# Performance work log

Hardware: AMD Instinct MI355X
Metric: run time of the kernel (lower is better)

The kernel has to match this reference:

```python
import jax, jax.numpy as jnp
import numpy as np

N, M = 1024, 1024
GATES = ["ii", "hi", "if", "hf", "ig", "hg", "io", "ho"]


def setup_inputs() -> dict:
    key = jax.random.key(0)
    names = ["x", "h", "c"] + [f"{p}_{g}" for g in GATES for p in ("L", "R", "b")]
    keys = jax.random.split(key, len(names))
    out = {}
    for nm, k in zip(names, keys):
        if nm in ("x", "h", "c"):
            sh = (N, M)
            scale = 1.0
        else:
            p = nm.split("_")[0]
            sh = {"L": (N, N), "R": (M, M), "b": (N, M)}[p]
            scale = 0.05  # keep gate pre-activations in a sane range
        out[nm] = jax.random.normal(k, sh, dtype=jnp.float32) * scale
    return out


def _klin(L, R, b, x):
    # kronecker_addmm: left @ x @ right + bias
    return L @ x @ R + b


def reference(x, h, c,
              L_ii, R_ii, b_ii, L_hi, R_hi, b_hi,
              L_if, R_if, b_if, L_hf, R_hf, b_hf,
              L_ig, R_ig, b_ig, L_hg, R_hg, b_hg,
              L_io, R_io, b_io, L_ho, R_ho, b_ho):
    i = jax.nn.sigmoid(_klin(L_ii, R_ii, b_ii, x) + _klin(L_hi, R_hi, b_hi, h))
    f = jax.nn.sigmoid(_klin(L_if, R_if, b_if, x) + _klin(L_hf, R_hf, b_hf, h))
    g = jnp.tanh(_klin(L_ig, R_ig, b_ig, x) + _klin(L_hg, R_hg, b_hg, h))
    o = jax.nn.sigmoid(_klin(L_io, R_io, b_io, x) + _klin(L_ho, R_ho, b_ho, h))
    c_new = f * c + i * g
    h_new = o * jnp.tanh(c_new)
    return (h_new, c_new)
```

## Files before the change

### kernel.cpp

```cpp
#include <hip/hip_runtime.h>
#include <stdint.h>

typedef __bf16 bf16x8 __attribute__((ext_vector_type(8)));
typedef float  f32x4  __attribute__((ext_vector_type(4)));
typedef uint16_t u16;

#define MAT_ELEMS (1024 * 1024)
#define LDK 1024


__device__ __forceinline__ u16 to_bf16(float f) {
  union { float f; uint32_t u; } v; v.f = f;
  uint32_t u = v.u;
  uint32_t r = u + 0x7FFFu + ((u >> 16) & 1u);
  return (u16)(r >> 16);
}

__device__ __forceinline__ void gll16(const void* g, void* l) {
  __builtin_amdgcn_global_load_lds(
      (__attribute__((address_space(1))) void*)const_cast<void*>(g),
      (__attribute__((address_space(3))) void*)(l),
      16, 0, 0);
}

__device__ __forceinline__ float fast_sigmoid(float x) {
  x = fminf(fmaxf(x, -30.f), 30.f);
  return 1.0f / (1.0f + __expf(-x));
}

__device__ __forceinline__ float fast_tanh(float x) {
  x = fminf(fmaxf(x, -15.f), 15.f);
  float e = __expf(2.0f * x);
  return (e - 1.0f) / (e + 1.0f);
}


struct P8  { const float* p[8]; };
struct P10 { const float* p[10]; };
struct B8  { const float* b[8]; };

__global__ __launch_bounds__(256) void cast8_kernel(P8 s, u16* __restrict__ dst) {
  const float* src = s.p[blockIdx.y];
  u16* d = dst + ((size_t)blockIdx.y << 20);
  int i = (blockIdx.x * 256 + threadIdx.x) * 4;
  f32x4 v = *reinterpret_cast<const f32x4*>(src + i);
  ushort4 o;
  o.x = to_bf16(v[0]); o.y = to_bf16(v[1]);
  o.z = to_bf16(v[2]); o.w = to_bf16(v[3]);
  *reinterpret_cast<ushort4*>(d + i) = o;
}

__global__ __launch_bounds__(256) void transpose_cast_kernel(P10 s, u16* __restrict__ dstbase) {
  __shared__ float tile[32][33];
  const float* src = s.p[blockIdx.z];
  u16* dst = dstbase + ((size_t)blockIdx.z << 20);
  int tx = threadIdx.x & 31;
  int ty = threadIdx.x >> 5;
  int c0 = blockIdx.x * 32;
  int r0 = blockIdx.y * 32;
#pragma unroll
  for (int i = 0; i < 4; ++i)
    tile[ty + i * 8][tx] = src[(size_t)(r0 + ty + i * 8) * 1024 + c0 + tx];
  __syncthreads();
#pragma unroll
  for (int i = 0; i < 4; ++i) {
    int n = c0 + ty + i * 8;
    int k = r0 + tx;
    dst[(size_t)n * 1024 + k] = to_bf16(tile[tx][ty + i * 8]);
  }
}


template <int MODE>
__device__ __forceinline__ void gemm_body(
    const u16* __restrict__ A0, const u16* __restrict__ A1,
    const u16* __restrict__ B0, const u16* __restrict__ B1,
    int nkt, int kt_split, int row0, int col0,
    u16* __restrict__ outb, float* __restrict__ outf,
    const float* __restrict__ bias0, const float* __restrict__ bias1,
    u16* As, u16* Bs)
{
  const int tid  = threadIdx.x;
  const int lane = tid & 63;
  const int w    = tid >> 6;
  const int wr   = w >> 1;
  const int wc   = w & 1;
  const int r16  = lane & 15;
  const int kg   = lane >> 4;

  f32x4 acc[4][4];
#pragma unroll
  for (int m = 0; m < 4; ++m)
#pragma unroll
    for (int n = 0; n < 4; ++n) {
      f32x4 z = {0.f, 0.f, 0.f, 0.f};
      acc[m][n] = z;
    }

  const int srow = tid >> 2;
  const int skk  = (tid & 3) * 8;
  u16* lA0 = As + srow * 32 + skk;
  u16* lA1 = As + (srow + 64) * 32 + skk;
  u16* lB0 = Bs + srow * 32 + skk;
  u16* lB1 = Bs + (srow + 64) * 32 + skk;

  for (int kt = 0; kt < nkt; ++kt) {
    const u16* Ak = (kt < kt_split) ? (A0 + kt * 32) : (A1 + (kt - kt_split) * 32);
    const u16* Bk = (kt < kt_split) ? (B0 + kt * 32) : (B1 + (kt - kt_split) * 32);
    __syncthreads();
    gll16(Ak + (size_t)(row0 + srow)      * LDK + skk, lA0);
    gll16(Ak + (size_t)(row0 + srow + 64) * LDK + skk, lA1);
    gll16(Bk + (size_t)(col0 + srow)      * LDK + skk, lB0);
    gll16(Bk + (size_t)(col0 + srow + 64) * LDK + skk, lB1);
    __syncthreads();

    bf16x8 af[4], bfr[4];
#pragma unroll
    for (int m = 0; m < 4; ++m)
      af[m] = *reinterpret_cast<const bf16x8*>(As + (wr * 64 + m * 16 + r16) * 32 + kg * 8);
#pragma unroll
    for (int n = 0; n < 4; ++n)
      bfr[n] = *reinterpret_cast<const bf16x8*>(Bs + (wc * 64 + n * 16 + r16) * 32 + kg * 8);
#pragma unroll
    for (int m = 0; m < 4; ++m)
#pragma unroll
      for (int n = 0; n < 4; ++n)
        acc[m][n] = __builtin_amdgcn_mfma_f32_16x16x32_bf16(af[m], bfr[n], acc[m][n], 0, 0, 0);
  }

#pragma unroll
  for (int m = 0; m < 4; ++m) {
#pragma unroll
    for (int r = 0; r < 4; ++r) {
      int row = row0 + wr * 64 + m * 16 + kg * 4 + r;
#pragma unroll
      for (int n = 0; n < 4; ++n) {
        int col = col0 + wc * 64 + n * 16 + r16;
        if (MODE == 0) {
          outb[(size_t)row * 1024 + col] = to_bf16(acc[m][n][r]);
        } else {
          size_t idx = (size_t)row * 1024 + col;
          outf[idx] = acc[m][n][r] + bias0[idx] + bias1[idx];
        }
      }
    }
  }
}

__global__ __launch_bounds__(256) void gemm_stage1_kernel(
    const u16* __restrict__ Lb, const u16* __restrict__ xT,
    const u16* __restrict__ hT, u16* __restrict__ Tbuf)
{
  __shared__ u16 As[128 * 32];
  __shared__ u16 Bs[128 * 32];
  int g = blockIdx.y;
  const u16* A = Lb + ((size_t)g << 20);
  const u16* B = (g & 1) ? hT : xT;
  u16* out = Tbuf + ((size_t)g << 20);
  int row0 = (blockIdx.x >> 3) * 128;
  int col0 = (blockIdx.x & 7) * 128;
  gemm_body<0>(A, A, B, B, 32, 32, row0, col0, out, nullptr, nullptr, nullptr, As, Bs);
}

__global__ __launch_bounds__(256) void gemm_stage2_kernel(
    const u16* __restrict__ Tbuf, const u16* __restrict__ RT,
    B8 bp, float* __restrict__ P)
{
  __shared__ u16 As[128 * 32];
  __shared__ u16 Bs[128 * 32];
  int j = blockIdx.y;
  const u16* A0 = Tbuf + ((size_t)(2 * j) << 20);
  const u16* B0 = RT   + ((size_t)(2 * j) << 20);
  int row0 = (blockIdx.x >> 3) * 128;
  int col0 = (blockIdx.x & 7) * 128;
  gemm_body<1>(A0, A0 + MAT_ELEMS, B0, B0 + MAT_ELEMS, 64, 32, row0, col0,
               nullptr, P + ((size_t)j << 20), bp.b[2 * j], bp.b[2 * j + 1], As, Bs);
}

__global__ __launch_bounds__(256) void lstm_cell_kernel(
    const float* __restrict__ P, const float* __restrict__ c, float* __restrict__ out)
{
  int i = (blockIdx.x * 256 + threadIdx.x) * 4;
  f32x4 pi = *reinterpret_cast<const f32x4*>(P + i);
  f32x4 pf = *reinterpret_cast<const f32x4*>(P + MAT_ELEMS + i);
  f32x4 pg = *reinterpret_cast<const f32x4*>(P + 2 * MAT_ELEMS + i);
  f32x4 po = *reinterpret_cast<const f32x4*>(P + 3 * MAT_ELEMS + i);
  f32x4 cc = *reinterpret_cast<const f32x4*>(c + i);
  f32x4 hn, cn;
#pragma unroll
  for (int j = 0; j < 4; ++j) {
    float ig = fast_sigmoid(pi[j]);
    float fg = fast_sigmoid(pf[j]);
    float gg = fast_tanh(pg[j]);
    float og = fast_sigmoid(po[j]);
    float cv = fg * cc[j] + ig * gg;
    cn[j] = cv;
    hn[j] = og * fast_tanh(cv);
  }
  *reinterpret_cast<f32x4*>(out + i) = hn;
  *reinterpret_cast<f32x4*>(out + MAT_ELEMS + i) = cn;
}


extern "C" void kernel_launch(void* const* d_in, const int* in_sizes, int n_in,
                              void* d_out, int out_size, void* d_ws, size_t ws_size,
                              hipStream_t stream) {
  const float* x = (const float*)d_in[0];
  const float* h = (const float*)d_in[1];
  const float* c = (const float*)d_in[2];

  u16* Lb   = (u16*)d_ws;
  u16* xT   = Lb + ((size_t)8 << 20);
  u16* hT   = xT + ((size_t)1 << 20);
  u16* RT   = hT + ((size_t)1 << 20);
  u16* Tbuf = RT + ((size_t)8 << 20);
  float* P  = (float*)(Tbuf + ((size_t)8 << 20));

  P8 lp;
  for (int g = 0; g < 8; ++g) lp.p[g] = (const float*)d_in[3 + 3 * g];
  P10 tp;
  tp.p[0] = x; tp.p[1] = h;
  for (int g = 0; g < 8; ++g) tp.p[2 + g] = (const float*)d_in[4 + 3 * g];
  B8 bp;
  for (int g = 0; g < 8; ++g) bp.b[g] = (const float*)d_in[5 + 3 * g];

  cast8_kernel<<<dim3(1024, 8), 256, 0, stream>>>(lp, Lb);
  transpose_cast_kernel<<<dim3(32, 32, 10), 256, 0, stream>>>(tp, xT);
  gemm_stage1_kernel<<<dim3(64, 8), 256, 0, stream>>>(Lb, xT, hT, Tbuf);
  gemm_stage2_kernel<<<dim3(64, 4), 256, 0, stream>>>(Tbuf, RT, bp, P);
  lstm_cell_kernel<<<1024, 256, 0, stream>>>(P, c, (float*)d_out);
}
```

Measured before the change: 258.0 us.

## Use 64x128 GEMM tiles and split stage-2 per gate with bf16 partials

Shrinks GEMM block tiles from 128x128 to 64x128, doubling block count in stage 1. Stage 2 no longer fuses the x and h products per gate into one 2048-deep reduction; it runs 8 independent 1024-deep GEMMs (1024 blocks instead of 256), each adding one bias and writing bf16. The LSTM cell kernel then reads 8 bf16 partials and sums the pairs. The goal is better CU occupancy on the many-CU device and less traffic for the intermediate P buffer. In exchange, each block reuses less data, the pre-activations lose precision, and the cell kernel reads more separate buffers.

Result: faster. 251.5 us (-2.5%).

```diff
diff --git a/kernel.cpp b/kernel.cpp
--- a/kernel.cpp
+++ b/kernel.cpp
@@ -14,6 +14,11 @@
   uint32_t u = v.u;
   uint32_t r = u + 0x7FFFu + ((u >> 16) & 1u);
   return (u16)(r >> 16);
+}
+
+__device__ __forceinline__ float bf16_to_f32(u16 b) {
+  union { uint32_t u; float f; } v; v.u = ((uint32_t)b) << 16;
+  return v.f;
 }
 
 __device__ __forceinline__ void gll16(const void* g, void* l) {
@@ -72,12 +77,10 @@
 
 
 template <int MODE>
-__device__ __forceinline__ void gemm_body(
-    const u16* __restrict__ A0, const u16* __restrict__ A1,
-    const u16* __restrict__ B0, const u16* __restrict__ B1,
-    int nkt, int kt_split, int row0, int col0,
-    u16* __restrict__ outb, float* __restrict__ outf,
-    const float* __restrict__ bias0, const float* __restrict__ bias1,
+__device__ __forceinline__ void gemm64_body(
+    const u16* __restrict__ A, const u16* __restrict__ B,
+    int row0, int col0,
+    u16* __restrict__ out, const float* __restrict__ bias,
     u16* As, u16* Bs)
 {
   const int tid  = threadIdx.x;
@@ -88,9 +91,9 @@
   const int r16  = lane & 15;
   const int kg   = lane >> 4;
 
-  f32x4 acc[4][4];
-#pragma unroll
-  for (int m = 0; m < 4; ++m)
+  f32x4 acc[2][4];
+#pragma unroll
+  for (int m = 0; m < 2; ++m)
 #pragma unroll
     for (int n = 0; n < 4; ++n) {
       f32x4 z = {0.f, 0.f, 0.f, 0.f};
@@ -99,49 +102,46 @@
 
   const int srow = tid >> 2;
   const int skk  = (tid & 3) * 8;
-  u16* lA0 = As + srow * 32 + skk;
-  u16* lA1 = As + (srow + 64) * 32 + skk;
+  u16* lA  = As + srow * 32 + skk;
   u16* lB0 = Bs + srow * 32 + skk;
   u16* lB1 = Bs + (srow + 64) * 32 + skk;
-
-  for (int kt = 0; kt < nkt; ++kt) {
-    const u16* Ak = (kt < kt_split) ? (A0 + kt * 32) : (A1 + (kt - kt_split) * 32);
-    const u16* Bk = (kt < kt_split) ? (B0 + kt * 32) : (B1 + (kt - kt_split) * 32);
+  const u16* gA  = A + (size_t)(row0 + srow)      * LDK + skk;
+  const u16* gB0 = B + (size_t)(col0 + srow)      * LDK + skk;
+  const u16* gB1 = B + (size_t)(col0 + srow + 64) * LDK + skk;
+
+  for (int kt = 0; kt < 32; ++kt) {
     __syncthreads();
-    gll16(Ak + (size_t)(row0 + srow)      * LDK + skk, lA0);
-    gll16(Ak + (size_t)(row0 + srow + 64) * LDK + skk, lA1);
-    gll16(Bk + (size_t)(col0 + srow)      * LDK + skk, lB0);
-    gll16(Bk + (size_t)(col0 + srow + 64) * LDK + skk, lB1);
+    gll16(gA  + kt * 32, lA);
+    gll16(gB0 + kt * 32, lB0);
+    gll16(gB1 + kt * 32, lB1);
     __syncthreads();
 
-    bf16x8 af[4], bfr[4];
-#pragma unroll
-    for (int m = 0; m < 4; ++m)
-      af[m] = *reinterpret_cast<const bf16x8*>(As + (wr * 64 + m * 16 + r16) * 32 + kg * 8);
+    bf16x8 af[2], bfr[4];
+#pragma unroll
+    for (int m = 0; m < 2; ++m)
+      af[m] = *reinterpret_cast<const bf16x8*>(As + (wr * 32 + m * 16 + r16) * 32 + kg * 8);
 #pragma unroll
     for (int n = 0; n < 4; ++n)
       bfr[n] = *reinterpret_cast<const bf16x8*>(Bs + (wc * 64 + n * 16 + r16) * 32 + kg * 8);
 #pragma unroll
-    for (int m = 0; m < 4; ++m)
+    for (int m = 0; m < 2; ++m)
 #pragma unroll
       for (int n = 0; n < 4; ++n)
         acc[m][n] = __builtin_amdgcn_mfma_f32_16x16x32_bf16(af[m], bfr[n], acc[m][n], 0, 0, 0);
   }
 
 #pragma unroll
-  for (int m = 0; m < 4; ++m) {
+  for (int m = 0; m < 2; ++m) {
 #pragma unroll
     for (int r = 0; r < 4; ++r) {
-      int row = row0 + wr * 64 + m * 16 + kg * 4 + r;
+      int row = row0 + wr * 32 + m * 16 + kg * 4 + r;
 #pragma unroll
       for (int n = 0; n < 4; ++n) {
         int col = col0 + wc * 64 + n * 16 + r16;
-        if (MODE == 0) {
-          outb[(size_t)row * 1024 + col] = to_bf16(acc[m][n][r]);
-        } else {
-          size_t idx = (size_t)row * 1024 + col;
-          outf[idx] = acc[m][n][r] + bias0[idx] + bias1[idx];
-        }
+        size_t idx = (size_t)row * 1024 + col;
+        float v = acc[m][n][r];
+        if (MODE == 1) v += bias[idx];
+        out[idx] = to_bf16(v);
       }
     }
   }
@@ -151,48 +151,50 @@
     const u16* __restrict__ Lb, const u16* __restrict__ xT,
     const u16* __restrict__ hT, u16* __restrict__ Tbuf)
 {
-  __shared__ u16 As[128 * 32];
+  __shared__ u16 As[64 * 32];
   __shared__ u16 Bs[128 * 32];
   int g = blockIdx.y;
   const u16* A = Lb + ((size_t)g << 20);
   const u16* B = (g & 1) ? hT : xT;
-  u16* out = Tbuf + ((size_t)g << 20);
-  int row0 = (blockIdx.x >> 3) * 128;
+  int row0 = (blockIdx.x >> 3) * 64;
   int col0 = (blockIdx.x & 7) * 128;
-  gemm_body<0>(A, A, B, B, 32, 32, row0, col0, out, nullptr, nullptr, nullptr, As, Bs);
+  gemm64_body<0>(A, B, row0, col0, Tbuf + ((size_t)g << 20), nullptr, As, Bs);
 }
 
 __global__ __launch_bounds__(256) void gemm_stage2_kernel(
     const u16* __restrict__ Tbuf, const u16* __restrict__ RT,
-    B8 bp, float* __restrict__ P)
-{
-  __shared__ u16 As[128 * 32];
+    B8 bp, u16* __restrict__ P)
+{
+  __shared__ u16 As[64 * 32];
   __shared__ u16 Bs[128 * 32];
-  int j = blockIdx.y;
-  const u16* A0 = Tbuf + ((size_t)(2 * j) << 20);
-  const u16* B0 = RT   + ((size_t)(2 * j) << 20);
-  int row0 = (blockIdx.x >> 3) * 128;
+  int g = blockIdx.y;
+  const u16* A = Tbuf + ((size_t)g << 20);
+  const u16* B = RT   + ((size_t)g << 20);
+  int row0 = (blockIdx.x >> 3) * 64;
   int col0 = (blockIdx.x & 7) * 128;
-  gemm_body<1>(A0, A0 + MAT_ELEMS, B0, B0 + MAT_ELEMS, 64, 32, row0, col0,
-               nullptr, P + ((size_t)j << 20), bp.b[2 * j], bp.b[2 * j + 1], As, Bs);
+  gemm64_body<1>(A, B, row0, col0, P + ((size_t)g << 20), bp.b[g], As, Bs);
 }
 
 __global__ __launch_bounds__(256) void lstm_cell_kernel(
-    const float* __restrict__ P, const float* __restrict__ c, float* __restrict__ out)
+    const u16* __restrict__ P, const float* __restrict__ c, float* __restrict__ out)
 {
   int i = (blockIdx.x * 256 + threadIdx.x) * 4;
-  f32x4 pi = *reinterpret_cast<const f32x4*>(P + i);
-  f32x4 pf = *reinterpret_cast<const f32x4*>(P + MAT_ELEMS + i);
-  f32x4 pg = *reinterpret_cast<const f32x4*>(P + 2 * MAT_ELEMS + i);
-  f32x4 po = *reinterpret_cast<const f32x4*>(P + 3 * MAT_ELEMS + i);
+  ushort4 pv[8];
+#pragma unroll
+  for (int g = 0; g < 8; ++g)
+    pv[g] = *reinterpret_cast<const ushort4*>(P + (size_t)g * MAT_ELEMS + i);
   f32x4 cc = *reinterpret_cast<const f32x4*>(c + i);
   f32x4 hn, cn;
 #pragma unroll
   for (int j = 0; j < 4; ++j) {
-    float ig = fast_sigmoid(pi[j]);
-    float fg = fast_sigmoid(pf[j]);
-    float gg = fast_tanh(pg[j]);
-    float og = fast_sigmoid(po[j]);
+    float pi = bf16_to_f32((&pv[0].x)[j]) + bf16_to_f32((&pv[1].x)[j]);
+    float pf = bf16_to_f32((&pv[2].x)[j]) + bf16_to_f32((&pv[3].x)[j]);
+    float pg = bf16_to_f32((&pv[4].x)[j]) + bf16_to_f32((&pv[5].x)[j]);
+    float po = bf16_to_f32((&pv[6].x)[j]) + bf16_to_f32((&pv[7].x)[j]);
+    float ig = fast_sigmoid(pi);
+    float fg = fast_sigmoid(pf);
+    float gg = fast_tanh(pg);
+    float og = fast_sigmoid(po);
     float cv = fg * cc[j] + ig * gg;
     cn[j] = cv;
     hn[j] = og * fast_tanh(cv);
@@ -214,7 +216,7 @@
   u16* hT   = xT + ((size_t)1 << 20);
   u16* RT   = hT + ((size_t)1 << 20);
   u16* Tbuf = RT + ((size_t)8 << 20);
-  float* P  = (float*)(Tbuf + ((size_t)8 << 20));
+  u16* P    = Tbuf + ((size_t)8 << 20);
 
   P8 lp;
   for (int g = 0; g < 8; ++g) lp.p[g] = (const float*)d_in[3 + 3 * g];
@@ -226,7 +228,7 @@
 
   cast8_kernel<<<dim3(1024, 8), 256, 0, stream>>>(lp, Lb);
   transpose_cast_kernel<<<dim3(32, 32, 10), 256, 0, stream>>>(tp, xT);
-  gemm_stage1_kernel<<<dim3(64, 8), 256, 0, stream>>>(Lb, xT, hT, Tbuf);
-  gemm_stage2_kernel<<<dim3(64, 4), 256, 0, stream>>>(Tbuf, RT, bp, P);
+  gemm_stage1_kernel<<<dim3(128, 8), 256, 0, stream>>>(Lb, xT, hT, Tbuf);
+  gemm_stage2_kernel<<<dim3(128, 8), 256, 0, stream>>>(Tbuf, RT, bp, P);
   lstm_cell_kernel<<<1024, 256, 0, stream>>>(P, c, (float*)d_out);
 }
```
